# Kernel tuning notes

Measured on AMD Instinct MI355X. Metric: run time of the kernel, lower is better.

Reference implementation:

```python
import jax, jax.numpy as jnp
import numpy as np

N_NODES, N_EDGES, D_IN, D_OUT = 50000, 800000, 64, 64
N_REL, N_TIME = 500, 1000


def setup_inputs() -> dict:
    key = jax.random.key(0)
    ks = jax.random.split(key, 14)
    xavier = lambda k, shape: jax.random.normal(k, shape, jnp.float32) * np.sqrt(2.0 / (shape[0] + shape[1])) * np.sqrt(2.0)
    return {
        "x": jax.random.normal(ks[0], (N_NODES, D_IN), jnp.float32),
        "rel_repr": jax.random.normal(ks[1], (N_REL, D_IN), jnp.float32),
        "time_emds": jax.random.normal(ks[2], (N_TIME, D_IN), jnp.float32),
        "src": jax.random.randint(ks[3], (N_EDGES,), 0, N_NODES),
        "dst": jax.random.randint(ks[4], (N_EDGES,), 0, N_NODES),
        "etype": jax.random.randint(ks[5], (N_EDGES,), 0, N_REL),
        "etime": jax.random.randint(ks[6], (N_EDGES,), 0, N_TIME),
        "trans_w": xavier(ks[7], (D_IN, D_OUT)),
        "loop_w": xavier(ks[8], (D_IN, D_OUT)),
        "w_rel": xavier(ks[9], (D_IN, D_OUT)),
        "attn_h": xavier(ks[10], (D_IN, 1)),
        "attn_t": xavier(ks[11], (D_IN, 1)),
        "attn_r": xavier(ks[12], (D_IN, 1)),
        "attn_ts": xavier(ks[13], (D_IN, 1)),
    }


def reference(x, rel_repr, time_emds, src, dst, etype, etime,
              trans_w, loop_w, w_rel, attn_h, attn_t, attn_r, attn_ts):
    n = x.shape[0]
    # per-node / per-rel / per-time scalar attention projections
    h_att = (x @ attn_h)[:, 0]          # [N]
    t_att = (x @ attn_t)[:, 0]          # [N]
    r_att = (rel_repr @ attn_r)[:, 0]   # [R]
    ts_att = (time_emds @ attn_ts)[:, 0]  # [T]
    # edge attention logits + edge_softmax grouped by destination node
    e = jax.nn.leaky_relu(h_att[src] - t_att[dst] + r_att[etype] + ts_att[etime], 0.1)  # [E]
    m = jax.ops.segment_max(e, dst, num_segments=n)
    ex = jnp.exp(e - m[dst])
    den = jax.ops.segment_sum(ex, dst, num_segments=n)
    att = (ex / den[dst])[:, None]      # [E,1]
    # message: (head + time) * (rel + time) -> trans_w -> weighted scatter-sum to dst
    time_emd = time_emds[etime]         # [E,D]
    edge_data = (x[src] + time_emd) * (rel_repr[etype] + time_emd)
    msg = (edge_data @ trans_w) * att   # [E,D_out]
    h = jax.ops.segment_sum(msg, dst, num_segments=n)
    x_out = h + x @ loop_w
    rel_out = rel_repr @ w_rel
    return (x_out, rel_out)
```

## Files before the change

kernel.cpp:

```cpp
#include <hip/hip_runtime.h>
#include <hip/hip_bf16.h>

#define N_NODES 50000
#define N_EDGES 800000
#define D 64
#define N_REL 500
#define N_TIME 1000
#define SLOTS 64
#define NODE_BLOCKS ((N_NODES + 63) / 64)
#define REL_BLOCKS  ((N_REL + 63) / 64)

#define NBUCKET 8
#define NODES_PER_BUCKET 6250
#define STAGE_CAP 131072
#define BIN_CAP 256
#define TILE 1024
#define PASS2_CHUNKS 128

__device__ __forceinline__ float bf2f(unsigned short u) {
    union { unsigned int i; float f; } v;
    v.i = ((unsigned int)u) << 16;
    return v.f;
}

__global__ void proj_kernel(const float* __restrict__ x,
                            const float* __restrict__ rel,
                            const float* __restrict__ tim,
                            const float* __restrict__ ah,
                            const float* __restrict__ at,
                            const float* __restrict__ ar,
                            const float* __restrict__ ats,
                            float* __restrict__ h_att, float* __restrict__ t_att,
                            float* __restrict__ r_att, float* __restrict__ ts_att,
                            unsigned short* __restrict__ x_bf) {
    int wave = (blockIdx.x * blockDim.x + threadIdx.x) >> 6;
    int lane = threadIdx.x & 63;
    const int total = N_NODES + N_REL + N_TIME;
    if (wave >= total) return;
    if (wave < N_NODES) {
        float xv = x[wave * D + lane];
        __hip_bfloat16 b = __float2bfloat16(xv);
        x_bf[wave * D + lane] = *(unsigned short*)&b;
        float s1 = xv * ah[lane];
        float s2 = xv * at[lane];
        for (int off = 32; off; off >>= 1) {
            s1 += __shfl_down(s1, off);
            s2 += __shfl_down(s2, off);
        }
        if (lane == 0) { h_att[wave] = s1; t_att[wave] = s2; }
    } else if (wave < N_NODES + N_REL) {
        int r = wave - N_NODES;
        float v = rel[r * D + lane] * ar[lane];
        for (int off = 32; off; off >>= 1) v += __shfl_down(v, off);
        if (lane == 0) r_att[r] = v;
    } else {
        int t = wave - N_NODES - N_REL;
        float v = tim[t * D + lane] * ats[lane];
        for (int off = 32; off; off >>= 1) v += __shfl_down(v, off);
        if (lane == 0) ts_att[t] = v;
    }
}

__global__ void build_kernel(const int* __restrict__ src, const int* __restrict__ dst,
                             const int* __restrict__ etype, const int* __restrict__ etime,
                             const float* __restrict__ h_att, const float* __restrict__ t_att,
                             const float* __restrict__ r_att, const float* __restrict__ ts_att,
                             int* __restrict__ cnt, int2* __restrict__ payload) {
    int e = blockIdx.x * blockDim.x + threadIdx.x;
    if (e >= N_EDGES) return;
    int s = src[e], d = dst[e], r = etype[e], t = etime[e];
    float lg = h_att[s] - t_att[d] + r_att[r] + ts_att[t];
    float lr = lg > 0.f ? lg : 0.1f * lg;
    float ex = __expf(lr);
    unsigned exb = __float_as_uint(ex);
    int2 pl;
    pl.x = (int)((exb & ~7u) | (unsigned)(s & 7));
    pl.y = (int)(((unsigned)(s >> 3) << 19) | ((unsigned)r << 10) | (unsigned)t);
    int pos = atomicAdd(&cnt[d], 1);
    if (pos < SLOTS) payload[(d << 6) + pos] = pl;
}

__global__ __launch_bounds__(256)
void bin_kernel(const int* __restrict__ src, const int* __restrict__ dst,
                const int* __restrict__ etype, const int* __restrict__ etime,
                const float* __restrict__ h_att, const float* __restrict__ t_att,
                const float* __restrict__ r_att, const float* __restrict__ ts_att,
                int* __restrict__ bucket_cursor, int4* __restrict__ stage) {
    __shared__ int4 bins[NBUCKET][BIN_CAP];
    __shared__ int bcnt[NBUCKET];
    __shared__ int bbase[NBUCKET];
    int t = threadIdx.x;
    if (t < NBUCKET) bcnt[t] = 0;
    __syncthreads();

    int e0 = blockIdx.x * TILE;
    for (int j = 0; j < 4; j++) {
        int e = e0 + j * 256 + t;
        if (e < N_EDGES) {
            int s = src[e], d = dst[e], r = etype[e], tt = etime[e];
            float lg = h_att[s] - t_att[d] + r_att[r] + ts_att[tt];
            float lr = lg > 0.f ? lg : 0.1f * lg;
            float ex = __expf(lr);
            unsigned exb = __float_as_uint(ex);
            int4 rec;
            rec.x = (int)((exb & ~7u) | (unsigned)(s & 7));
            rec.y = (int)(((unsigned)(s >> 3) << 19) | ((unsigned)r << 10) | (unsigned)tt);
            rec.z = d;
            rec.w = 0;
            int k = (int)((unsigned)d / NODES_PER_BUCKET);
            int pos = atomicAdd(&bcnt[k], 1);
            if (pos < BIN_CAP) {
                bins[k][pos] = rec;
            } else {
                int g = atomicAdd(&bucket_cursor[k], 1);
                if (g < STAGE_CAP) stage[k * STAGE_CAP + g] = rec;
            }
        }
    }
    __syncthreads();
    if (t < NBUCKET) {
        int c = bcnt[t] < BIN_CAP ? bcnt[t] : BIN_CAP;
        bbase[t] = atomicAdd(&bucket_cursor[t], c);
        bcnt[t] = c;
    }
    __syncthreads();
    for (int k = 0; k < NBUCKET; k++) {
        int c = bcnt[k];
        int base = bbase[k];
        for (int idx = t; idx < c; idx += 256) {
            int g = base + idx;
            if (g < STAGE_CAP) stage[k * STAGE_CAP + g] = bins[k][idx];
        }
    }
}

__global__ __launch_bounds__(256)
void scatter_kernel(const int* __restrict__ bucket_cursor,
                    const int4* __restrict__ stage,
                    int* __restrict__ cnt, int2* __restrict__ payload) {
    int b = blockIdx.x & (NBUCKET - 1);
    int chunk = blockIdx.x >> 3;
    int n = bucket_cursor[b];
    if (n > STAGE_CAP) n = STAGE_CAP;
    int ch = (n + PASS2_CHUNKS - 1) / PASS2_CHUNKS;
    int start = chunk * ch;
    int end = start + ch;
    if (end > n) end = n;
    for (int idx = start + (int)threadIdx.x; idx < end; idx += 256) {
        int4 rec = stage[b * STAGE_CAP + idx];
        int d = rec.z;
        int pos = atomicAdd(&cnt[d], 1);
        if (pos < SLOTS) payload[(d << 6) + pos] = make_int2(rec.x, rec.y);
    }
}

__global__ void node_gather_kernel(const unsigned short* __restrict__ x_bf,
                                   const float* __restrict__ rel,
                                   const float* __restrict__ tim,
                                   const int* __restrict__ cnt,
                                   const int2* __restrict__ payload,
                                   float* __restrict__ agg) {
    int d = (blockIdx.x * blockDim.x + threadIdx.x) >> 6;
    int lane = threadIdx.x & 63;
    if (d >= N_NODES) return;
    int deg = cnt[d];
    if (deg > SLOTS) deg = SLOTS;

    int s_l = 0, r_l = 0, t_l = 0;
    float ex = 0.f;
    if (lane < deg) {
        int2 pl = payload[(d << 6) + lane];
        unsigned px = (unsigned)pl.x;
        unsigned py = (unsigned)pl.y;
        ex = __uint_as_float(px & ~7u);
        s_l = (int)(((py >> 19) << 3) | (px & 7u));
        r_l = (int)((py >> 10) & 511u);
        t_l = (int)(py & 1023u);
    }
    float den = ex;
    for (int off = 32; off; off >>= 1) den += __shfl_xor(den, off);
    float att_l = (lane < deg) ? ex / den : 0.f;

    int qw = lane >> 4;
    int ql = lane & 15;
    float4 acc = make_float4(0.f, 0.f, 0.f, 0.f);
    for (int i = 0; i < deg; i += 4) {
        int ei = i + qw;
        int s = __shfl(s_l, ei);
        int r = __shfl(r_l, ei);
        int t = __shfl(t_l, ei);
        float att = __shfl(att_l, ei);
        float4  te = *(const float4*)(tim + t * D + ql * 4);
        ushort4 xb = *(const ushort4*)(x_bf + s * D + ql * 4);
        float4  rl = *(const float4*)(rel + r * D + ql * 4);
        acc.x += att * (bf2f(xb.x) + te.x) * (rl.x + te.x);
        acc.y += att * (bf2f(xb.y) + te.y) * (rl.y + te.y);
        acc.z += att * (bf2f(xb.z) + te.z) * (rl.z + te.z);
        acc.w += att * (bf2f(xb.w) + te.w) * (rl.w + te.w);
    }
    for (int off = 16; off <= 32; off <<= 1) {
        acc.x += __shfl_xor(acc.x, off);
        acc.y += __shfl_xor(acc.y, off);
        acc.z += __shfl_xor(acc.z, off);
        acc.w += __shfl_xor(acc.w, off);
    }
    if (qw == 0)
        *(float4*)(agg + (d << 7) + ql * 4) = acc;
}

__global__ __launch_bounds__(256, 4)
void out_gemm_kernel(const float* __restrict__ agg,
                     const float* __restrict__ x,
                     const float* __restrict__ rel,
                     const float* __restrict__ trans_w,
                     const float* __restrict__ loop_w,
                     const float* __restrict__ w_rel,
                     float* __restrict__ out) {
    __shared__ float Wa[D * D];
    __shared__ float Wb[D * D];
    int t = threadIdx.x;
    bool nodeb = blockIdx.x < NODE_BLOCKS;

    for (int j = 0; j < 4; j++) {
        int idx = (t + 256 * j) * 4;
        if (nodeb) {
            *(float4*)(Wa + idx) = *(const float4*)(trans_w + idx);
            *(float4*)(Wb + idx) = *(const float4*)(loop_w + idx);
        } else {
            *(float4*)(Wa + idx) = *(const float4*)(w_rel + idx);
        }
    }
    __syncthreads();

    int lane = t & 63;
    int wv = t >> 6;
    int c4 = (lane & 15) << 2;
    int r0 = wv * 16 + (lane >> 4) * 4;

    float acc[4][4];
    for (int i = 0; i < 4; i++)
        for (int c = 0; c < 4; c++) acc[i][c] = 0.f;

    if (nodeb) {
        int row0 = blockIdx.x * 64;
        for (int k = 0; k < D; k += 4) {
            float wt[4][4], wl[4][4];
            for (int kk = 0; kk < 4; kk++) {
                *(float4*)&wt[kk][0] = *(const float4*)(Wa + (k + kk) * D + c4);
                *(float4*)&wl[kk][0] = *(const float4*)(Wb + (k + kk) * D + c4);
            }
            for (int i = 0; i < 4; i++) {
                int gr = row0 + r0 + i;
                if (gr >= N_NODES) gr = N_NODES - 1;
                float a[4], xv[4];
                *(float4*)&a[0]  = *(const float4*)(agg + (size_t)gr * 128 + k);
                *(float4*)&xv[0] = *(const float4*)(x   + (size_t)gr * D + k);
                for (int c = 0; c < 4; c++) {
                    float s = acc[i][c];
                    for (int kk = 0; kk < 4; kk++)
                        s += a[kk] * wt[kk][c] + xv[kk] * wl[kk][c];
                    acc[i][c] = s;
                }
            }
        }
        for (int i = 0; i < 4; i++) {
            int gr = row0 + r0 + i;
            if (gr < N_NODES)
                *(float4*)(out + (size_t)gr * D + c4) = *(float4*)&acc[i][0];
        }
    } else {
        int row0 = (blockIdx.x - NODE_BLOCKS) * 64;
        for (int k = 0; k < D; k += 4) {
            float wt[4][4];
            for (int kk = 0; kk < 4; kk++)
                *(float4*)&wt[kk][0] = *(const float4*)(Wa + (k + kk) * D + c4);
            for (int i = 0; i < 4; i++) {
                int gr = row0 + r0 + i;
                if (gr >= N_REL) gr = N_REL - 1;
                float a[4];
                *(float4*)&a[0] = *(const float4*)(rel + (size_t)gr * D + k);
                for (int c = 0; c < 4; c++) {
                    float s = acc[i][c];
                    for (int kk = 0; kk < 4; kk++)
                        s += a[kk] * wt[kk][c];
                    acc[i][c] = s;
                }
            }
        }
        for (int i = 0; i < 4; i++) {
            int gr = row0 + r0 + i;
            if (gr < N_REL)
                *(float4*)(out + (size_t)(N_NODES + gr) * D + c4) = *(float4*)&acc[i][0];
        }
    }
}

extern "C" void kernel_launch(void* const* d_in, const int* in_sizes, int n_in,
                              void* d_out, int out_size, void* d_ws, size_t ws_size,
                              hipStream_t stream) {
    const float* x    = (const float*)d_in[0];
    const float* rel  = (const float*)d_in[1];
    const float* tim  = (const float*)d_in[2];
    const int* src   = (const int*)d_in[3];
    const int* dst   = (const int*)d_in[4];
    const int* etype = (const int*)d_in[5];
    const int* etime = (const int*)d_in[6];
    const float* trans_w = (const float*)d_in[7];
    const float* loop_w  = (const float*)d_in[8];
    const float* w_rel   = (const float*)d_in[9];
    const float* ah  = (const float*)d_in[10];
    const float* at  = (const float*)d_in[11];
    const float* ar  = (const float*)d_in[12];
    const float* ats = (const float*)d_in[13];

    char* ws = (char*)d_ws;
    int*   cnt            = (int*)  (ws);
    int*   bucket_cursor  = (int*)  (ws + 200000);
    float* h_att          = (float*)(ws + 200064);
    float* t_att          = (float*)(ws + 400064);
    float* r_att          = (float*)(ws + 600064);
    float* ts_att         = (float*)(ws + 602064);
    int2*  payload        = (int2*) (ws + 1000000);
    float* agg            = (float*)(ws + 1000000);
    unsigned short* x_bf  = (unsigned short*)(ws + 26600000);
    int4*  stage          = (int4*) (ws + 33000000);

    float* out = (float*)d_out;

    const size_t need = 33000000ull + (size_t)NBUCKET * STAGE_CAP * sizeof(int4);
    const bool two_phase = (ws_size >= need);

    hipMemsetAsync(cnt, 0, 200032, stream);

    {
        int waves = N_NODES + N_REL + N_TIME;
        proj_kernel<<<(waves + 3) / 4, 256, 0, stream>>>(
            x, rel, tim, ah, at, ar, ats,
            h_att, t_att, r_att, ts_att, x_bf);
    }
    if (two_phase) {
        bin_kernel<<<(N_EDGES + TILE - 1) / TILE, 256, 0, stream>>>(
            src, dst, etype, etime, h_att, t_att, r_att, ts_att,
            bucket_cursor, stage);
        scatter_kernel<<<NBUCKET * PASS2_CHUNKS, 256, 0, stream>>>(
            bucket_cursor, stage, cnt, payload);
    } else {
        build_kernel<<<(N_EDGES + 255) / 256, 256, 0, stream>>>(
            src, dst, etype, etime, h_att, t_att, r_att, ts_att, cnt, payload);
    }
    {
        node_gather_kernel<<<(N_NODES + 3) / 4, 256, 0, stream>>>(
            x_bf, rel, tim, cnt, payload, agg);
    }
    {
        out_gemm_kernel<<<NODE_BLOCKS + REL_BLOCKS, 256, 0, stream>>>(
            agg, x, rel, trans_w, loop_w, w_rel, out);
    }
}
```

Before: 219.3 us.

## Bin edges into fine node buckets and fuse the scatter into the gather

Edges are now binned by 128-node destination bucket into a per-bucket staging area. A new fused node kernel has each block read its bucket, sort the records into per-node shared-memory slots with shared atomics, then run the softmax and weighted gather directly. This removes the separate scatter kernel, its global per-node atomics and the round trip through the global payload array. It also compacts the agg stride to 64. In exchange, each bucket is read by two blocks, the bin kernel uses about 50KB of shared memory, and each node keeps at most 48 edges.

```diff
diff --git a/kernel.cpp b/kernel.cpp
--- a/kernel.cpp
+++ b/kernel.cpp
@@ -10,12 +10,14 @@
 #define NODE_BLOCKS ((N_NODES + 63) / 64)
 #define REL_BLOCKS  ((N_REL + 63) / 64)
 
-#define NBUCKET 8
-#define NODES_PER_BUCKET 6250
-#define STAGE_CAP 131072
-#define BIN_CAP 256
-#define TILE 1024
-#define PASS2_CHUNKS 128
+#define CB 128
+#define NCB ((N_NODES + CB - 1) / CB)
+#define FR 64
+#define NFB ((N_NODES + FR - 1) / FR)
+#define SCAP 4096
+#define BINCAP 8
+#define BTILE 1024
+#define LSLOT 48
 
 __device__ __forceinline__ float bf2f(unsigned short u) {
     union { unsigned int i; float f; } v;
@@ -61,6 +63,136 @@
     }
 }
 
+__global__ __launch_bounds__(256)
+void bin_kernel(const int* __restrict__ src, const int* __restrict__ dst,
+                const int* __restrict__ etype, const int* __restrict__ etime,
+                const float* __restrict__ h_att, const float* __restrict__ t_att,
+                const float* __restrict__ r_att, const float* __restrict__ ts_att,
+                int* __restrict__ cursor, int4* __restrict__ stage) {
+    __shared__ int4 bins[NCB][BINCAP];
+    __shared__ int bcnt[NCB];
+    int t = threadIdx.x;
+    for (int k = t; k < NCB; k += 256) bcnt[k] = 0;
+    __syncthreads();
+
+    int e0 = blockIdx.x * BTILE;
+    for (int j = 0; j < 4; j++) {
+        int e = e0 + j * 256 + t;
+        if (e < N_EDGES) {
+            int s = src[e], d = dst[e], r = etype[e], tt = etime[e];
+            float lg = h_att[s] - t_att[d] + r_att[r] + ts_att[tt];
+            float lr = lg > 0.f ? lg : 0.1f * lg;
+            float ex = __expf(lr);
+            unsigned exb = __float_as_uint(ex);
+            int4 rec;
+            rec.x = (int)((exb & ~7u) | (unsigned)(s & 7));
+            rec.y = (int)(((unsigned)(s >> 3) << 19) | ((unsigned)r << 10) | (unsigned)tt);
+            rec.z = d;
+            rec.w = 0;
+            int k = d >> 7;
+            int pos = atomicAdd(&bcnt[k], 1);
+            if (pos < BINCAP) {
+                bins[k][pos] = rec;
+            } else {
+                int g = atomicAdd(&cursor[k], 1);
+                if (g < SCAP) stage[(size_t)k * SCAP + g] = rec;
+            }
+        }
+    }
+    __syncthreads();
+    for (int k = t; k < NCB; k += 256) {
+        int c = bcnt[k];
+        if (c > BINCAP) c = BINCAP;
+        if (c > 0) {
+            int base = atomicAdd(&cursor[k], c);
+            for (int i = 0; i < c; i++) {
+                int g = base + i;
+                if (g < SCAP) stage[(size_t)k * SCAP + g] = bins[k][i];
+            }
+        }
+    }
+}
+
+__global__ __launch_bounds__(256)
+void node_fused_kernel(const unsigned short* __restrict__ x_bf,
+                       const float* __restrict__ rel,
+                       const float* __restrict__ tim,
+                       const int* __restrict__ cursor,
+                       const int4* __restrict__ stage,
+                       float* __restrict__ agg) {
+    __shared__ int2 lslot[FR * LSLOT];
+    __shared__ int lcnt[FR];
+    int tid = threadIdx.x;
+    int base = blockIdx.x * FR;
+    int pb = blockIdx.x >> 1;
+
+    for (int i = tid; i < FR; i += 256) lcnt[i] = 0;
+    __syncthreads();
+
+    int n = cursor[pb];
+    if (n > SCAP) n = SCAP;
+    for (int i = tid; i < n; i += 256) {
+        int4 rec = stage[(size_t)pb * SCAP + i];
+        int ln = rec.z - base;
+        if ((unsigned)ln < FR) {
+            int pos = atomicAdd(&lcnt[ln], 1);
+            if (pos < LSLOT) lslot[ln * LSLOT + pos] = make_int2(rec.x, rec.y);
+        }
+    }
+    __syncthreads();
+
+    int lane = tid & 63;
+    int wv = tid >> 6;
+    int qw = lane >> 4;
+    int ql = lane & 15;
+
+    for (int ln = wv; ln < FR; ln += 4) {
+        int d = base + ln;
+        if (d >= N_NODES) break;
+        int deg = lcnt[ln];
+        if (deg > LSLOT) deg = LSLOT;
+
+        int s_l = 0, r_l = 0, t_l = 0;
+        float ex = 0.f;
+        if (lane < deg) {
+            int2 pl = lslot[ln * LSLOT + lane];
+            unsigned px = (unsigned)pl.x;
+            unsigned py = (unsigned)pl.y;
+            ex = __uint_as_float(px & ~7u);
+            s_l = (int)(((py >> 19) << 3) | (px & 7u));
+            r_l = (int)((py >> 10) & 511u);
+            t_l = (int)(py & 1023u);
+        }
+        float den = ex;
+        for (int off = 32; off; off >>= 1) den += __shfl_xor(den, off);
+        float att_l = (lane < deg) ? ex / den : 0.f;
+
+        float4 acc = make_float4(0.f, 0.f, 0.f, 0.f);
+        for (int i = 0; i < deg; i += 4) {
+            int ei = i + qw;
+            int s = __shfl(s_l, ei);
+            int r = __shfl(r_l, ei);
+            int t = __shfl(t_l, ei);
+            float att = __shfl(att_l, ei);
+            float4  te = *(const float4*)(tim + t * D + ql * 4);
+            ushort4 xb = *(const ushort4*)(x_bf + s * D + ql * 4);
+            float4  rl = *(const float4*)(rel + r * D + ql * 4);
+            acc.x += att * (bf2f(xb.x) + te.x) * (rl.x + te.x);
+            acc.y += att * (bf2f(xb.y) + te.y) * (rl.y + te.y);
+            acc.z += att * (bf2f(xb.z) + te.z) * (rl.z + te.z);
+            acc.w += att * (bf2f(xb.w) + te.w) * (rl.w + te.w);
+        }
+        for (int off = 16; off <= 32; off <<= 1) {
+            acc.x += __shfl_xor(acc.x, off);
+            acc.y += __shfl_xor(acc.y, off);
+            acc.z += __shfl_xor(acc.z, off);
+            acc.w += __shfl_xor(acc.w, off);
+        }
+        if (qw == 0)
+            *(float4*)(agg + (size_t)d * D + ql * 4) = acc;
+    }
+}
+
 __global__ void build_kernel(const int* __restrict__ src, const int* __restrict__ dst,
                              const int* __restrict__ etype, const int* __restrict__ etime,
                              const float* __restrict__ h_att, const float* __restrict__ t_att,
@@ -80,80 +212,6 @@
     if (pos < SLOTS) payload[(d << 6) + pos] = pl;
 }
 
-__global__ __launch_bounds__(256)
-void bin_kernel(const int* __restrict__ src, const int* __restrict__ dst,
-                const int* __restrict__ etype, const int* __restrict__ etime,
-                const float* __restrict__ h_att, const float* __restrict__ t_att,
-                const float* __restrict__ r_att, const float* __restrict__ ts_att,
-                int* __restrict__ bucket_cursor, int4* __restrict__ stage) {
-    __shared__ int4 bins[NBUCKET][BIN_CAP];
-    __shared__ int bcnt[NBUCKET];
-    __shared__ int bbase[NBUCKET];
-    int t = threadIdx.x;
-    if (t < NBUCKET) bcnt[t] = 0;
-    __syncthreads();
-
-    int e0 = blockIdx.x * TILE;
-    for (int j = 0; j < 4; j++) {
-        int e = e0 + j * 256 + t;
-        if (e < N_EDGES) {
-            int s = src[e], d = dst[e], r = etype[e], tt = etime[e];
-            float lg = h_att[s] - t_att[d] + r_att[r] + ts_att[tt];
-            float lr = lg > 0.f ? lg : 0.1f * lg;
-            float ex = __expf(lr);
-            unsigned exb = __float_as_uint(ex);
-            int4 rec;
-            rec.x = (int)((exb & ~7u) | (unsigned)(s & 7));
-            rec.y = (int)(((unsigned)(s >> 3) << 19) | ((unsigned)r << 10) | (unsigned)tt);
-            rec.z = d;
-            rec.w = 0;
-            int k = (int)((unsigned)d / NODES_PER_BUCKET);
-            int pos = atomicAdd(&bcnt[k], 1);
-            if (pos < BIN_CAP) {
-                bins[k][pos] = rec;
-            } else {
-                int g = atomicAdd(&bucket_cursor[k], 1);
-                if (g < STAGE_CAP) stage[k * STAGE_CAP + g] = rec;
-            }
-        }
-    }
-    __syncthreads();
-    if (t < NBUCKET) {
-        int c = bcnt[t] < BIN_CAP ? bcnt[t] : BIN_CAP;
-        bbase[t] = atomicAdd(&bucket_cursor[t], c);
-        bcnt[t] = c;
-    }
-    __syncthreads();
-    for (int k = 0; k < NBUCKET; k++) {
-        int c = bcnt[k];
-        int base = bbase[k];
-        for (int idx = t; idx < c; idx += 256) {
-            int g = base + idx;
-            if (g < STAGE_CAP) stage[k * STAGE_CAP + g] = bins[k][idx];
-        }
-    }
-}
-
-__global__ __launch_bounds__(256)
-void scatter_kernel(const int* __restrict__ bucket_cursor,
-                    const int4* __restrict__ stage,
-                    int* __restrict__ cnt, int2* __restrict__ payload) {
-    int b = blockIdx.x & (NBUCKET - 1);
-    int chunk = blockIdx.x >> 3;
-    int n = bucket_cursor[b];
-    if (n > STAGE_CAP) n = STAGE_CAP;
-    int ch = (n + PASS2_CHUNKS - 1) / PASS2_CHUNKS;
-    int start = chunk * ch;
-    int end = start + ch;
-    if (end > n) end = n;
-    for (int idx = start + (int)threadIdx.x; idx < end; idx += 256) {
-        int4 rec = stage[b * STAGE_CAP + idx];
-        int d = rec.z;
-        int pos = atomicAdd(&cnt[d], 1);
-        if (pos < SLOTS) payload[(d << 6) + pos] = make_int2(rec.x, rec.y);
-    }
-}
-
 __global__ void node_gather_kernel(const unsigned short* __restrict__ x_bf,
                                    const float* __restrict__ rel,
                                    const float* __restrict__ tim,
@@ -165,7 +223,6 @@
     if (d >= N_NODES) return;
     int deg = cnt[d];
     if (deg > SLOTS) deg = SLOTS;
-
     int s_l = 0, r_l = 0, t_l = 0;
     float ex = 0.f;
     if (lane < deg) {
@@ -180,7 +237,6 @@
     float den = ex;
     for (int off = 32; off; off >>= 1) den += __shfl_xor(den, off);
     float att_l = (lane < deg) ? ex / den : 0.f;
-
     int qw = lane >> 4;
     int ql = lane & 15;
     float4 acc = make_float4(0.f, 0.f, 0.f, 0.f);
@@ -215,7 +271,7 @@
                      const float* __restrict__ trans_w,
                      const float* __restrict__ loop_w,
                      const float* __restrict__ w_rel,
-                     float* __restrict__ out) {
+                     float* __restrict__ out, int astride) {
     __shared__ float Wa[D * D];
     __shared__ float Wb[D * D];
     int t = threadIdx.x;
@@ -253,7 +309,7 @@
                 int gr = row0 + r0 + i;
                 if (gr >= N_NODES) gr = N_NODES - 1;
                 float a[4], xv[4];
-                *(float4*)&a[0]  = *(const float4*)(agg + (size_t)gr * 128 + k);
+                *(float4*)&a[0]  = *(const float4*)(agg + (size_t)gr * astride + k);
                 *(float4*)&xv[0] = *(const float4*)(x   + (size_t)gr * D + k);
                 for (int c = 0; c < 4; c++) {
                     float s = acc[i][c];
@@ -314,23 +370,23 @@
     const float* ats = (const float*)d_in[13];
 
     char* ws = (char*)d_ws;
+    int*   cursor         = (int*)  (ws);
     int*   cnt            = (int*)  (ws);
-    int*   bucket_cursor  = (int*)  (ws + 200000);
     float* h_att          = (float*)(ws + 200064);
     float* t_att          = (float*)(ws + 400064);
     float* r_att          = (float*)(ws + 600064);
     float* ts_att         = (float*)(ws + 602064);
+    float* agg            = (float*)(ws + 1000000);
     int2*  payload        = (int2*) (ws + 1000000);
-    float* agg            = (float*)(ws + 1000000);
     unsigned short* x_bf  = (unsigned short*)(ws + 26600000);
     int4*  stage          = (int4*) (ws + 33000000);
 
     float* out = (float*)d_out;
 
-    const size_t need = 33000000ull + (size_t)NBUCKET * STAGE_CAP * sizeof(int4);
-    const bool two_phase = (ws_size >= need);
-
-    hipMemsetAsync(cnt, 0, 200032, stream);
+    const size_t need = 33000000ull + (size_t)NCB * SCAP * sizeof(int4);
+    const bool fused = (ws_size >= need);
+
+    hipMemsetAsync(ws, 0, 200000, stream);
 
     {
         int waves = N_NODES + N_REL + N_TIME;
@@ -338,22 +394,20 @@
             x, rel, tim, ah, at, ar, ats,
             h_att, t_att, r_att, ts_att, x_bf);
     }
-    if (two_phase) {
-        bin_kernel<<<(N_EDGES + TILE - 1) / TILE, 256, 0, stream>>>(
+    if (fused) {
+        bin_kernel<<<(N_EDGES + BTILE - 1) / BTILE, 256, 0, stream>>>(
             src, dst, etype, etime, h_att, t_att, r_att, ts_att,
-            bucket_cursor, stage);
-        scatter_kernel<<<NBUCKET * PASS2_CHUNKS, 256, 0, stream>>>(
-            bucket_cursor, stage, cnt, payload);
+            cursor, stage);
+        node_fused_kernel<<<NFB, 256, 0, stream>>>(
+            x_bf, rel, tim, cursor, stage, agg);
+        out_gemm_kernel<<<NODE_BLOCKS + REL_BLOCKS, 256, 0, stream>>>(
+            agg, x, rel, trans_w, loop_w, w_rel, out, 64);
     } else {
         build_kernel<<<(N_EDGES + 255) / 256, 256, 0, stream>>>(
             src, dst, etype, etime, h_att, t_att, r_att, ts_att, cnt, payload);
-    }
-    {
         node_gather_kernel<<<(N_NODES + 3) / 4, 256, 0, stream>>>(
             x_bf, rel, tim, cnt, payload, agg);
-    }
-    {
         out_gemm_kernel<<<NODE_BLOCKS + REL_BLOCKS, 256, 0, stream>>>(
-            agg, x, rel, trans_w, loop_w, w_rel, out);
-    }
-}
+            agg, x, rel, trans_w, loop_w, w_rel, out, 128);
+    }
+}
```

New measurement: 214.0 us. -2.4%, faster.
